# Kernel tuning notes

Measured on AMD Instinct MI355X. Metric: run time of the kernel, lower is better.

The kernel has to match this reference:

```python
import jax, jax.numpy as jnp
import numpy as np

# NanGradSkip is identity in forward (backward replaces NaN grads with 0)
@jax.custom_vjp
def nan_grad_skip(x):
    return x

def _ngs_fwd(x):
    return x, None

def _ngs_bwd(_, g):
    return (jnp.where(jnp.isnan(g), jnp.zeros_like(g), g),)

nan_grad_skip.defvjp(_ngs_fwd, _ngs_bwd)


def setup_inputs() -> dict:
    key = jax.random.key(0)
    # x > 0 so the log2 LUT path is well-defined (FixedRangeObserver limits analog)
    x = jax.random.uniform(key, (32, 4096, 1024), dtype=jnp.float32) * 4.0 + 0.25
    alpha = jnp.float32(1.0)                 # VIMul imm (2**(q_addr-q_rem) when quantized)
    falpha = jnp.float32(-np.log2(1.0))      # VIMul imm = -f(alpha)
    return {"x": x, "alpha": alpha, "falpha": falpha, "shamt": 0}


def reference(x, alpha, falpha, shamt):
    # function f with additive identity f(a*b) = f(a) + f(b)
    f = jnp.log2
    x = nan_grad_skip(x)
    # shift_down: addr = x >> shamt  (float sim: multiply by 2^-shamt)
    addr = x * jnp.asarray(2.0 ** (-shamt), x.dtype)
    # gt0 -> is_large; is_small = 1 + (-is_large)
    is_large = (addr > 0).astype(x.dtype)
    is_small = 1.0 - is_large
    # shift_rem: shamt = -1 -> rem = x * 2; then VIMul by alpha
    rem = (x * 2.0) * alpha
    # mux: mixed_addr = addr*is_large + rem*is_small
    mixed_addr = addr * is_large + rem * is_small
    # BareLUT(f)
    mixed_y = f(mixed_addr)
    # is_small_shift (shamt=0, identity) then VIMul by falpha = -f(alpha)
    to_add = falpha * is_small
    # demixer VVAdd
    return mixed_y + to_add
```

## Files before the change

kernel.cpp:

```cpp
#include <hip/hip_runtime.h>
#include <hip/hip_bf16.h>


__global__ __launch_bounds__(256) void addid_tlut_kernel(
    const float* __restrict__ x,
    float* __restrict__ out,
    const float* __restrict__ alpha_p,
    const float* __restrict__ falpha_p,
    const int* __restrict__ shamt_p,
    long long n)
{
    const float alpha  = *alpha_p;
    const float falpha = *falpha_p;
    const int   shamt  = *shamt_p;
    const float scale  = exp2f((float)(-shamt));

    long long i4   = (long long)blockIdx.x * blockDim.x + threadIdx.x;
    long long base = i4 * 4;
    if (base >= n) return;

    if (base + 3 < n) {
        float4 v = *reinterpret_cast<const float4*>(x + base);
        float4 r;
        {
            float xv = v.x;
            float addr = xv * scale;
            bool large = addr > 0.0f;
            float mixed = large ? addr : (xv * 2.0f) * alpha;
            float y = __log2f(mixed);
            r.x = large ? y : y + falpha;
        }
        {
            float xv = v.y;
            float addr = xv * scale;
            bool large = addr > 0.0f;
            float mixed = large ? addr : (xv * 2.0f) * alpha;
            float y = __log2f(mixed);
            r.y = large ? y : y + falpha;
        }
        {
            float xv = v.z;
            float addr = xv * scale;
            bool large = addr > 0.0f;
            float mixed = large ? addr : (xv * 2.0f) * alpha;
            float y = __log2f(mixed);
            r.z = large ? y : y + falpha;
        }
        {
            float xv = v.w;
            float addr = xv * scale;
            bool large = addr > 0.0f;
            float mixed = large ? addr : (xv * 2.0f) * alpha;
            float y = __log2f(mixed);
            r.w = large ? y : y + falpha;
        }
        *reinterpret_cast<float4*>(out + base) = r;
    } else {
        for (long long j = base; j < n; ++j) {
            float xv = x[j];
            float addr = xv * scale;
            bool large = addr > 0.0f;
            float mixed = large ? addr : (xv * 2.0f) * alpha;
            float y = __log2f(mixed);
            out[j] = large ? y : y + falpha;
        }
    }
}

extern "C" void kernel_launch(void* const* d_in, const int* in_sizes, int n_in,
                              void* d_out, int out_size, void* d_ws, size_t ws_size,
                              hipStream_t stream) {
    const float* x        = (const float*)d_in[0];
    const float* alpha_p  = (const float*)d_in[1];
    const float* falpha_p = (const float*)d_in[2];
    const int*   shamt_p  = (const int*)d_in[3];
    float* out = (float*)d_out;

    long long n = (long long)in_sizes[0];
    long long n4 = (n + 3) / 4;
    int block = 256;
    long long grid = (n4 + block - 1) / block;

    addid_tlut_kernel<<<(dim3)(unsigned)grid, block, 0, stream>>>(
        x, out, alpha_p, falpha_p, shamt_p, n);
}
```

Baseline: 815.1 us.

## Use grid-stride loop with 4x unroll and nontemporal vector loads/stores

Replaces the one-thread-per-float4 launch with a grid capped at 2048 blocks that walks the array in a grid-stride loop. Each iteration issues four independent float4 loads before computing. Loads and stores now use nontemporal builtins so the streaming data does not pollute caches. This is meant to raise memory-level parallelism and cut block scheduling overhead for a purely bandwidth-bound op, but the capped grid risks leaving some CUs underused and nontemporal hints can behave differently on CDNA.

```diff
diff --git a/kernel.cpp b/kernel.cpp
--- a/kernel.cpp
+++ b/kernel.cpp
@@ -1,6 +1,26 @@
 #include <hip/hip_runtime.h>
-#include <hip/hip_bf16.h>
 
+
+typedef float f32x4 __attribute__((ext_vector_type(4)));
+
+__device__ __forceinline__ float addid_op(float xv, float scale, float alpha, float falpha)
+{
+    float addr  = xv * scale;
+    bool  large = addr > 0.0f;
+    float mixed = large ? addr : (xv * 2.0f) * alpha;
+    float y     = __log2f(mixed);
+    return large ? y : y + falpha;
+}
+
+__device__ __forceinline__ f32x4 addid_op4(f32x4 v, float scale, float alpha, float falpha)
+{
+    f32x4 r;
+    r.x = addid_op(v.x, scale, alpha, falpha);
+    r.y = addid_op(v.y, scale, alpha, falpha);
+    r.z = addid_op(v.z, scale, alpha, falpha);
+    r.w = addid_op(v.w, scale, alpha, falpha);
+    return r;
+}
 
 __global__ __launch_bounds__(256) void addid_tlut_kernel(
     const float* __restrict__ x,
@@ -15,72 +35,61 @@
     const int   shamt  = *shamt_p;
     const float scale  = exp2f((float)(-shamt));
 
-    long long i4   = (long long)blockIdx.x * blockDim.x + threadIdx.x;
-    long long base = i4 * 4;
-    if (base >= n) return;
+    const long long n4  = n >> 2;
+    const long long nth = (long long)gridDim.x * blockDim.x;
+    const long long tid = (long long)blockIdx.x * blockDim.x + threadIdx.x;
 
-    if (base + 3 < n) {
-        float4 v = *reinterpret_cast<const float4*>(x + base);
-        float4 r;
-        {
-            float xv = v.x;
-            float addr = xv * scale;
-            bool large = addr > 0.0f;
-            float mixed = large ? addr : (xv * 2.0f) * alpha;
-            float y = __log2f(mixed);
-            r.x = large ? y : y + falpha;
-        }
-        {
-            float xv = v.y;
-            float addr = xv * scale;
-            bool large = addr > 0.0f;
-            float mixed = large ? addr : (xv * 2.0f) * alpha;
-            float y = __log2f(mixed);
-            r.y = large ? y : y + falpha;
-        }
-        {
-            float xv = v.z;
-            float addr = xv * scale;
-            bool large = addr > 0.0f;
-            float mixed = large ? addr : (xv * 2.0f) * alpha;
-            float y = __log2f(mixed);
-            r.z = large ? y : y + falpha;
-        }
-        {
-            float xv = v.w;
-            float addr = xv * scale;
-            bool large = addr > 0.0f;
-            float mixed = large ? addr : (xv * 2.0f) * alpha;
-            float y = __log2f(mixed);
-            r.w = large ? y : y + falpha;
-        }
-        *reinterpret_cast<float4*>(out + base) = r;
-    } else {
-        for (long long j = base; j < n; ++j) {
-            float xv = x[j];
-            float addr = xv * scale;
-            bool large = addr > 0.0f;
-            float mixed = large ? addr : (xv * 2.0f) * alpha;
-            float y = __log2f(mixed);
-            out[j] = large ? y : y + falpha;
-        }
+    const f32x4* __restrict__ xv = reinterpret_cast<const f32x4*>(x);
+    f32x4* __restrict__ ov       = reinterpret_cast<f32x4*>(out);
+
+    long long i = tid;
+
+    for (; i + 3 * nth < n4; i += 4 * nth) {
+        f32x4 v0 = __builtin_nontemporal_load(xv + i);
+        f32x4 v1 = __builtin_nontemporal_load(xv + i + nth);
+        f32x4 v2 = __builtin_nontemporal_load(xv + i + 2 * nth);
+        f32x4 v3 = __builtin_nontemporal_load(xv + i + 3 * nth);
+
+        f32x4 r0 = addid_op4(v0, scale, alpha, falpha);
+        f32x4 r1 = addid_op4(v1, scale, alpha, falpha);
+        f32x4 r2 = addid_op4(v2, scale, alpha, falpha);
+        f32x4 r3 = addid_op4(v3, scale, alpha, falpha);
+
+        __builtin_nontemporal_store(r0, ov + i);
+        __builtin_nontemporal_store(r1, ov + i + nth);
+        __builtin_nontemporal_store(r2, ov + i + 2 * nth);
+        __builtin_nontemporal_store(r3, ov + i + 3 * nth);
+    }
+
+    for (; i < n4; i += nth) {
+        f32x4 v = __builtin_nontemporal_load(xv + i);
+        __builtin_nontemporal_store(addid_op4(v, scale, alpha, falpha), ov + i);
+    }
+
+    if (tid == 0) {
+        for (long long j = (n4 << 2); j < n; ++j)
+            out[j] = addid_op(x[j], scale, alpha, falpha);
     }
 }
 
 extern "C" void kernel_launch(void* const* d_in, const int* in_sizes, int n_in,
                               void* d_out, int out_size, void* d_ws, size_t ws_size,
-                              hipStream_t stream) {
+                              hipStream_t stream)
+{
     const float* x        = (const float*)d_in[0];
     const float* alpha_p  = (const float*)d_in[1];
     const float* falpha_p = (const float*)d_in[2];
     const int*   shamt_p  = (const int*)d_in[3];
     float* out = (float*)d_out;
 
-    long long n = (long long)in_sizes[0];
-    long long n4 = (n + 3) / 4;
-    int block = 256;
-    long long grid = (n4 + block - 1) / block;
+    long long n  = (long long)in_sizes[0];
+    long long n4 = n >> 2;
+    const int block = 256;
 
-    addid_tlut_kernel<<<(dim3)(unsigned)grid, block, 0, stream>>>(
+    long long want = (n4 + block - 1) / block;
+    if (want < 1) want = 1;
+    unsigned grid = (unsigned)((want < 2048) ? want : 2048);
+
+    addid_tlut_kernel<<<dim3(grid), dim3(block), 0, stream>>>(
         x, out, alpha_p, falpha_p, shamt_p, n);
 }
```

After: 888.7 us. 9.0% more time.
